# Optimization experiments

Measured on AMD Instinct MI355X. Metric: run time of the kernel, lower is better.

Reference implementation:

```python
import jax, jax.numpy as jnp
import numpy as np

B, S, E, L = 4, 4096, 1024, 64
SCALE = float(np.sqrt(L))


def setup_inputs() -> dict:
    key = jax.random.key(0)
    ks = jax.random.split(key, 7)
    x = jax.random.normal(ks[0], (B, S, E), dtype=jnp.float32)
    # causal mask: positions with mask==0 are disallowed (masked_fill semantics)
    mask = jnp.tril(jnp.ones((S, S), dtype=jnp.int32))
    # Linear params (torch Linear: y = x @ W.T + b); store as [E, L] for x @ W
    sd = 1.0 / np.sqrt(E)
    Wq = jax.random.uniform(ks[1], (E, L), jnp.float32, -sd, sd)
    Wk = jax.random.uniform(ks[2], (E, L), jnp.float32, -sd, sd)
    Wv = jax.random.uniform(ks[3], (E, L), jnp.float32, -sd, sd)
    bq = jax.random.uniform(ks[4], (L,), jnp.float32, -sd, sd)
    bk = jax.random.uniform(ks[5], (L,), jnp.float32, -sd, sd)
    bv = jax.random.uniform(ks[6], (L,), jnp.float32, -sd, sd)
    return {"x": x, "Wq": Wq, "Wk": Wk, "Wv": Wv,
            "bq": bq, "bk": bk, "bv": bv, "mask": mask}


def reference(x, Wq, Wk, Wv, bq, bk, bv, mask):
    # Q,K,V: [B, S, L]
    Q = x @ Wq + bq
    K = x @ Wk + bk
    V = x @ Wv + bv
    # scores: [B, S, S] -- naive full matrix, faithful to the original
    scores = jnp.einsum('bsl,btl->bst', Q, K) / SCALE
    scores = jnp.where(mask == 0, -jnp.inf, scores)
    attn = jax.nn.softmax(scores, axis=-1)
    return jnp.einsum('bst,btl->bsl', attn, V)
```

## Files before the change

### kernel.cpp

```cpp
#include <hip/hip_runtime.h>
#include <hip/hip_bf16.h>
#include <cstdint>

typedef __bf16 bf16_t;
typedef __bf16 bf16x8 __attribute__((ext_vector_type(8)));
typedef float f32x4 __attribute__((ext_vector_type(4)));

#define B_ 4
#define S_ 4096
#define E_ 1024
#define L_ 64

__device__ __forceinline__ f32x4 mfma16(bf16x8 a, bf16x8 b, f32x4 c) {
  return __builtin_amdgcn_mfma_f32_16x16x32_bf16(a, b, c, 0, 0, 0);
}

__device__ __forceinline__ void barrier_lds_only() {
  asm volatile("s_waitcnt lgkmcnt(0)\n\ts_barrier" ::: "memory");
}

template <int CTRL>
__device__ __forceinline__ float dpp_max_step(float x) {
  int t = __builtin_amdgcn_update_dpp(0, __float_as_int(x), CTRL, 0xF, 0xF, true);
  return fmaxf(x, __int_as_float(t));
}
template <int CTRL>
__device__ __forceinline__ float dpp_add_step(float x) {
  int t = __builtin_amdgcn_update_dpp(0, __float_as_int(x), CTRL, 0xF, 0xF, true);
  return x + __int_as_float(t);
}
__device__ __forceinline__ float dpp_reduce_max16(float x) {
  x = dpp_max_step<0x121>(x);
  x = dpp_max_step<0x122>(x);
  x = dpp_max_step<0x124>(x);
  x = dpp_max_step<0x128>(x);
  return x;
}
__device__ __forceinline__ float dpp_reduce_add16(float x) {
  x = dpp_add_step<0x121>(x);
  x = dpp_add_step<0x122>(x);
  x = dpp_add_step<0x124>(x);
  x = dpp_add_step<0x128>(x);
  return x;
}


__global__ void prep_w_kernel(const float* __restrict__ Wq, const float* __restrict__ Wk,
                              const float* __restrict__ Wv, bf16_t* __restrict__ Wf) {
  int n = blockIdx.x >> 1;
  int k0 = (blockIdx.x & 1) * 512;
  const float* W = (n < 64) ? Wq : (n < 128 ? Wk : Wv);
  int col = n & 63;
  int nt = n >> 4, lr = n & 15;
  for (int kk = threadIdx.x; kk < 512; kk += blockDim.x) {
    int k = k0 + kk;
    int kt = k >> 5, lg = (k >> 3) & 3, e = k & 7;
    Wf[((size_t)((nt * 32 + kt) * 64 + lg * 16 + lr) << 3) + e] = (bf16_t)W[(size_t)k * L_ + col];
  }
}

__global__ __launch_bounds__(512) void qkv_proj_kernel(
    const float* __restrict__ x, const bf16_t* __restrict__ Wf,
    const float* __restrict__ bq, const float* __restrict__ bk, const float* __restrict__ bv,
    bf16_t* __restrict__ Qf, bf16_t* __restrict__ Kf, bf16_t* __restrict__ Vf) {
  __shared__ __align__(16) bf16_t xbuf[2][32][136];
  bf16_t* stc = &xbuf[0][0][0];

  const int tid = threadIdx.x;
  const int w = tid >> 6, l = tid & 63;
  const int lr = l & 15, lg = l >> 4;
  const int rowgrp = w & 1, colgrp = w >> 1;
  const int m0 = blockIdx.x * 32;
  const int rot = blockIdx.x & 7;

  const int prow = tid >> 4;
  const int pcol = (tid & 15) * 8;
  float4 ra, rb;

#define QKV_CC(c) (((c) + rot) & 7)
#define QKV_LOADREG(c)                                                      \
  {                                                                         \
    const float* src = x + (size_t)(m0 + prow) * E_ + QKV_CC(c) * 128 + pcol; \
    ra = *reinterpret_cast<const float4*>(src);                             \
    rb = *reinterpret_cast<const float4*>(src + 4);                         \
  }
#define QKV_WRITE(b)                                                        \
  {                                                                         \
    bf16x8 pk;                                                              \
    pk[0] = (bf16_t)ra.x; pk[1] = (bf16_t)ra.y;                             \
    pk[2] = (bf16_t)ra.z; pk[3] = (bf16_t)ra.w;                             \
    pk[4] = (bf16_t)rb.x; pk[5] = (bf16_t)rb.y;                             \
    pk[6] = (bf16_t)rb.z; pk[7] = (bf16_t)rb.w;                             \
    *reinterpret_cast<bf16x8*>(&xbuf[(b)][prow][pcol]) = pk;                \
  }

  f32x4 acc[3];
#pragma unroll
  for (int t = 0; t < 3; ++t) acc[t] = f32x4{0.f, 0.f, 0.f, 0.f};

  QKV_LOADREG(0);
  QKV_WRITE(0);
  QKV_LOADREG(1);
  barrier_lds_only();

  for (int c = 0; c < 8; ++c) {
    const int cur = c & 1;
    const int cc = QKV_CC(c);
#pragma unroll
    for (int kt = 0; kt < 4; ++kt) {
      const int ktg = cc * 4 + kt;
      bf16x8 bfr[3];
#pragma unroll
      for (int t = 0; t < 3; ++t) {
        const int nt = colgrp * 3 + t;
        bfr[t] = *reinterpret_cast<const bf16x8*>(Wf + (((size_t)(nt * 32 + ktg) * 64 + l) << 3));
      }
      bf16x8 a = *reinterpret_cast<const bf16x8*>(
          &xbuf[cur][rowgrp * 16 + lr][kt * 32 + lg * 8]);
#pragma unroll
      for (int t = 0; t < 3; ++t) acc[t] = mfma16(a, bfr[t], acc[t]);
    }
    if (c + 1 < 8) QKV_WRITE(cur ^ 1);
    if (c + 2 < 8) QKV_LOADREG(c + 2);
    barrier_lds_only();
  }

#pragma unroll
  for (int t = 0; t < 3; ++t) {
    const int colb = colgrp * 48 + t * 16;
    const int col = colb + lr;
    const int mat = colb >> 6;
    const float* bias = (mat == 0) ? bq : (mat == 1 ? bk : bv);
    const float bb = bias[col & 63];
#pragma unroll
    for (int r = 0; r < 4; ++r) {
      const int row = rowgrp * 16 + lg * 4 + r;
      stc[row * 200 + col] = (bf16_t)(acc[t][r] + bb);
    }
  }
  __syncthreads();

  if (tid < 256) {
    const int rt = tid >> 7, ktq = (tid >> 6) & 1, lane = tid & 63;
    const int lgw = lane >> 4, lrw = lane & 15;
    const int rtg = (m0 >> 4) + rt;
    bf16x8 qv = *reinterpret_cast<const bf16x8*>(stc + (rt * 16 + lrw) * 200 + ktq * 32 + lgw * 8);
    *reinterpret_cast<bf16x8*>(Qf + (((size_t)(rtg * 2 + ktq) * 64 + lane) << 3)) = qv;
    bf16x8 kv = *reinterpret_cast<const bf16x8*>(stc + (rt * 16 + lrw) * 200 + 64 + ktq * 32 + lgw * 8);
    *reinterpret_cast<bf16x8*>(Kf + (((size_t)(rtg * 2 + ktq) * 64 + lane) << 3)) = kv;
  } else {
    const int t2 = tid - 256;
    const int vt = t2 >> 6, lane = t2 & 63;
    const int lgv = lane >> 4, lrv = lane & 15;
    const int colv = vt * 16 + lrv;
    bf16x8 vv;
#pragma unroll
    for (int e = 0; e < 8; ++e)
      vv[e] = stc[(lgv * 8 + e) * 200 + 128 + colv];
    const int batch = m0 >> 12;
    const int stg = (m0 & (S_ - 1)) >> 5;
    *reinterpret_cast<bf16x8*>(Vf + ((size_t)batch << 18) + (((size_t)(stg * 4 + vt) * 64 + lane) << 3)) = vv;
  }
#undef QKV_CC
#undef QKV_LOADREG
#undef QKV_WRITE
}

__global__ __launch_bounds__(256) void attn_kernel(
    const bf16_t* __restrict__ Qf, const bf16_t* __restrict__ Kf,
    const bf16_t* __restrict__ Vf, bf16_t* __restrict__ Opart, float* __restrict__ mlpart) {
  __shared__ __align__(16) bf16_t p_lds[4][16 * 72];
  __shared__ bf16_t od_lds[3][16][68];
  __shared__ float ml_lds[3][16][2];

  const int c = threadIdx.x >> 6, l = threadIdx.x & 63;
  const int lr = l & 15, lg = l >> 4;
  const int u = blockIdx.x;
  const int batch = u & 3;
  const int strip = (u >> 2) & 3;
  const int h = (u >> 4) & 1;
  const int qt = 63 - (u >> 5);
  const int qsi = ((u >> 5) << 4) | (u & 15);
  const int qrow = qt * 64 + strip * 16;
  bf16_t* pw = p_lds[c];

  const int rtq = batch * 256 + qt * 4 + strip;
  bf16x8 qa0 = *reinterpret_cast<const bf16x8*>(Qf + (((size_t)(rtq * 2) * 64 + l) << 3));
  bf16x8 qa1 = *reinterpret_cast<const bf16x8*>(Qf + (((size_t)(rtq * 2 + 1) * 64 + l) << 3));
  const bf16_t* Vb = Vf + ((size_t)batch << 18);

  f32x4 o[4];
  float m[4], ssum[4];
#pragma unroll
  for (int rr = 0; rr < 4; ++rr) { o[rr] = f32x4{0.f, 0.f, 0.f, 0.f}; m[rr] = -1e30f; ssum[rr] = 0.f; }

  for (int kt = 2 * c + h; kt <= qt; kt += 8) {
    const int t0 = kt * 64;
    f32x4 st[4];
#pragma unroll
    for (int cf = 0; cf < 4; ++cf) st[cf] = f32x4{0.f, 0.f, 0.f, 0.f};
#pragma unroll
    for (int cf = 0; cf < 4; ++cf) {
      const int rtk = batch * 256 + kt * 4 + cf;
      bf16x8 b0 = *reinterpret_cast<const bf16x8*>(Kf + (((size_t)(rtk * 2) * 64 + l) << 3));
      bf16x8 b1 = *reinterpret_cast<const bf16x8*>(Kf + (((size_t)(rtk * 2 + 1) * 64 + l) << 3));
      st[cf] = mfma16(qa0, b0, st[cf]);
      st[cf] = mfma16(qa1, b1, st[cf]);
    }
    const bool diag = (kt == qt);
    float p[4][4];
#pragma unroll
    for (int rr = 0; rr < 4; ++rr) {
      const int qg = qrow + lg * 4 + rr;
      float rowmax = -1e30f;
#pragma unroll
      for (int cf = 0; cf < 4; ++cf) {
        float s = st[cf][rr] * 0.125f;
        if (diag && (t0 + cf * 16 + lr) > qg) s = -1e30f;
        p[cf][rr] = s;
        rowmax = fmaxf(rowmax, s);
      }
      rowmax = dpp_reduce_max16(rowmax);
      float mnew = fmaxf(m[rr], rowmax);
      float scale = __expf(m[rr] - mnew);
      float rs = 0.f;
#pragma unroll
      for (int cf = 0; cf < 4; ++cf) {
        float e = __expf(p[cf][rr] - mnew);
        p[cf][rr] = e;
        rs += e;
      }
      rs = dpp_reduce_add16(rs);
      ssum[rr] = ssum[rr] * scale + rs;
#pragma unroll
      for (int cf = 0; cf < 4; ++cf) o[cf][rr] *= scale;
      m[rr] = mnew;
    }
#pragma unroll
    for (int rr = 0; rr < 4; ++rr)
#pragma unroll
      for (int cf = 0; cf < 4; ++cf)
        pw[(lg * 4 + rr) * 72 + cf * 16 + lr] = (bf16_t)p[cf][rr];
    bf16x8 pa0 = *reinterpret_cast<const bf16x8*>(pw + lr * 72 + lg * 8);
    bf16x8 pa1 = *reinterpret_cast<const bf16x8*>(pw + lr * 72 + 32 + lg * 8);
    const int st0 = kt * 2;
#pragma unroll
    for (int cf = 0; cf < 4; ++cf) {
      bf16x8 v0 = *reinterpret_cast<const bf16x8*>(Vb + (((size_t)((st0 * 4 + cf) * 64 + l)) << 3));
      bf16x8 v1 = *reinterpret_cast<const bf16x8*>(Vb + (((size_t)(((st0 + 1) * 4 + cf) * 64 + l)) << 3));
      o[cf] = mfma16(pa0, v0, o[cf]);
      o[cf] = mfma16(pa1, v1, o[cf]);
    }
  }

  if (c > 0) {
    if (lr == 0) {
#pragma unroll
      for (int rr = 0; rr < 4; ++rr) {
        ml_lds[c - 1][lg * 4 + rr][0] = m[rr];
        ml_lds[c - 1][lg * 4 + rr][1] = ssum[rr];
      }
    }
#pragma unroll
    for (int cf = 0; cf < 4; ++cf)
#pragma unroll
      for (int rr = 0; rr < 4; ++rr)
        od_lds[c - 1][lg * 4 + rr][cf * 16 + lr] = (bf16_t)o[cf][rr];
  }
  __syncthreads();
  if (c == 0) {
    bf16_t* Op = Opart + (size_t)(h * 1024 + qsi) * 1024;
    float* mlp = mlpart + (size_t)(h * 1024 + qsi) * 32;
#pragma unroll
    for (int rr = 0; rr < 4; ++rr) {
      const int row = lg * 4 + rr;
      float M = m[rr];
      float mv[3];
#pragma unroll
      for (int cc = 0; cc < 3; ++cc) {
        mv[cc] = ml_lds[cc][row][0];
        M = fmaxf(M, mv[cc]);
      }
      float f0 = __expf(m[rr] - M);
      float Lsum = ssum[rr] * f0;
      float fc[3];
#pragma unroll
      for (int cc = 0; cc < 3; ++cc) {
        fc[cc] = __expf(mv[cc] - M);
        Lsum += ml_lds[cc][row][1] * fc[cc];
      }
      const float invL = (Lsum > 0.f) ? (1.f / Lsum) : 0.f;
      if (lr == 0) { mlp[row * 2] = M; mlp[row * 2 + 1] = Lsum; }
#pragma unroll
      for (int cf = 0; cf < 4; ++cf) {
        float val = o[cf][rr] * f0;
#pragma unroll
        for (int cc = 0; cc < 3; ++cc)
          val += (float)od_lds[cc][row][cf * 16 + lr] * fc[cc];
        Op[row * 64 + cf * 16 + lr] = (bf16_t)(val * invL);
      }
    }
  }
}

__global__ __launch_bounds__(64) void combine_kernel(
    const bf16_t* __restrict__ Opart, const float* __restrict__ mlpart,
    float* __restrict__ out) {
  const int b = blockIdx.x;
  const int batch = b & 3, strip = (b >> 2) & 3, qt = 63 - (b >> 4);
  const int l = threadIdx.x;
  const int row = l >> 2, c0 = (l & 3) * 16;
  const float* ml0 = mlpart + ((size_t)(0 * 1024 + b) * 16 + row) * 2;
  const float* ml1 = mlpart + ((size_t)(1 * 1024 + b) * 16 + row) * 2;
  float m0 = ml0[0], l0 = ml0[1], m1 = ml1[0], l1 = ml1[1];
  float M = fmaxf(m0, m1);
  float w0 = l0 * __expf(m0 - M), w1 = l1 * __expf(m1 - M);
  float inv = 1.f / (w0 + w1);
  w0 *= inv; w1 *= inv;
  const bf16_t* O0 = Opart + (size_t)(0 * 1024 + b) * 1024 + row * 64 + c0;
  const bf16_t* O1 = Opart + (size_t)(1 * 1024 + b) * 1024 + row * 64 + c0;
  float* dst = out + ((size_t)batch * S_ + qt * 64 + strip * 16 + row) * L_ + c0;
#pragma unroll
  for (int j = 0; j < 2; ++j) {
    bf16x8 a = reinterpret_cast<const bf16x8*>(O0)[j];
    bf16x8 bb = reinterpret_cast<const bf16x8*>(O1)[j];
#pragma unroll
    for (int e = 0; e < 8; ++e)
      dst[j * 8 + e] = (float)a[e] * w0 + (float)bb[e] * w1;
  }
}

extern "C" void kernel_launch(void* const* d_in, const int* in_sizes, int n_in,
                              void* d_out, int out_size, void* d_ws, size_t ws_size,
                              hipStream_t stream) {
  (void)in_sizes; (void)n_in; (void)out_size; (void)ws_size;
  const float* x  = (const float*)d_in[0];
  const float* Wq = (const float*)d_in[1];
  const float* Wk = (const float*)d_in[2];
  const float* Wv = (const float*)d_in[3];
  const float* bq = (const float*)d_in[4];
  const float* bk = (const float*)d_in[5];
  const float* bv = (const float*)d_in[6];
  float* out = (float*)d_out;

  char* ws = (char*)d_ws;
  bf16_t* Qf  = (bf16_t*)(ws + 0);
  bf16_t* Kf  = (bf16_t*)(ws + (size_t)2 * 1024 * 1024);
  bf16_t* Vf  = (bf16_t*)(ws + (size_t)4 * 1024 * 1024);
  bf16_t* Wf  = (bf16_t*)(ws + (size_t)6 * 1024 * 1024);
  bf16_t* Opart = (bf16_t*)(ws + (size_t)7 * 1024 * 1024);
  float* mlpart = (float*)(ws + (size_t)12 * 1024 * 1024);

  hipLaunchKernelGGL(prep_w_kernel, dim3(384), dim3(256), 0, stream, Wq, Wk, Wv, Wf);
  hipLaunchKernelGGL(qkv_proj_kernel, dim3(16384 / 32), dim3(512), 0, stream,
                     x, Wf, bq, bk, bv, Qf, Kf, Vf);
  hipLaunchKernelGGL(attn_kernel, dim3(2048), dim3(256), 0, stream,
                     Qf, Kf, Vf, Opart, mlpart);
  hipLaunchKernelGGL(combine_kernel, dim3(1024), dim3(64), 0, stream,
                     Opart, mlpart, out);
}
```

Before: 59.39 us.

## Pre-cast x to bf16 in MFMA fragment layout via separate kernel

Adds an xcast kernel that converts x from fp32 to bf16 and writes it in the MFMA A-fragment layout. The QKV projection then reads A fragments straight from global memory, with no LDS double buffering and no per-chunk barriers. This removes the cast and sync work from the projection's inner loop. In exchange it adds a kernel launch and an extra 32MB round trip for the bf16 copy of x (read 64MB fp32, write 32MB, then read 32MB again), which is likely to cost more than it saves for a memory-bound stage.

```diff
diff --git a/kernel.cpp b/kernel.cpp
--- a/kernel.cpp
+++ b/kernel.cpp
@@ -13,10 +13,6 @@
 
 __device__ __forceinline__ f32x4 mfma16(bf16x8 a, bf16x8 b, f32x4 c) {
   return __builtin_amdgcn_mfma_f32_16x16x32_bf16(a, b, c, 0, 0, 0);
-}
-
-__device__ __forceinline__ void barrier_lds_only() {
-  asm volatile("s_waitcnt lgkmcnt(0)\n\ts_barrier" ::: "memory");
 }
 
 template <int CTRL>
@@ -44,6 +40,39 @@
   return x;
 }
 
+
+__global__ __launch_bounds__(256) void xcast_kernel(
+    const float* __restrict__ x, bf16_t* __restrict__ xf) {
+  __shared__ __align__(16) bf16_t xs[16][1048];
+  const int tid = threadIdx.x;
+  const int m0 = blockIdx.x * 16;
+  {
+    const float* xb = x + (size_t)m0 * E_;
+#pragma unroll
+    for (int p = 0; p < 8; ++p) {
+      const int g = p * 256 + tid;
+      const int row = g >> 7, col = (g & 127) * 8;
+      float4 u0 = *reinterpret_cast<const float4*>(xb + (size_t)row * E_ + col);
+      float4 u1 = *reinterpret_cast<const float4*>(xb + (size_t)row * E_ + col + 4);
+      bf16x8 pk;
+      pk[0] = (bf16_t)u0.x; pk[1] = (bf16_t)u0.y; pk[2] = (bf16_t)u0.z; pk[3] = (bf16_t)u0.w;
+      pk[4] = (bf16_t)u1.x; pk[5] = (bf16_t)u1.y; pk[6] = (bf16_t)u1.z; pk[7] = (bf16_t)u1.w;
+      *reinterpret_cast<bf16x8*>(&xs[row][col]) = pk;
+    }
+  }
+  __syncthreads();
+  {
+    const int rt = m0 >> 4;
+#pragma unroll
+    for (int i = 0; i < 8; ++i) {
+      const int idx = i * 256 + tid;
+      const int lane = idx & 63, kt = idx >> 6;
+      const int lrw = lane & 15, lgw = lane >> 4;
+      bf16x8 v = *reinterpret_cast<const bf16x8*>(&xs[lrw][kt * 32 + lgw * 8]);
+      *reinterpret_cast<bf16x8*>(xf + (((size_t)(rt * 32 + kt) * 64 + lane) << 3)) = v;
+    }
+  }
+}
 
 __global__ void prep_w_kernel(const float* __restrict__ Wq, const float* __restrict__ Wk,
                               const float* __restrict__ Wv, bf16_t* __restrict__ Wf) {
@@ -60,69 +89,32 @@
 }
 
 __global__ __launch_bounds__(512) void qkv_proj_kernel(
-    const float* __restrict__ x, const bf16_t* __restrict__ Wf,
+    const bf16_t* __restrict__ xf, const bf16_t* __restrict__ Wf,
     const float* __restrict__ bq, const float* __restrict__ bk, const float* __restrict__ bv,
     bf16_t* __restrict__ Qf, bf16_t* __restrict__ Kf, bf16_t* __restrict__ Vf) {
-  __shared__ __align__(16) bf16_t xbuf[2][32][136];
-  bf16_t* stc = &xbuf[0][0][0];
+  __shared__ __align__(16) bf16_t stc[32 * 200];
 
   const int tid = threadIdx.x;
   const int w = tid >> 6, l = tid & 63;
   const int lr = l & 15, lg = l >> 4;
   const int rowgrp = w & 1, colgrp = w >> 1;
   const int m0 = blockIdx.x * 32;
-  const int rot = blockIdx.x & 7;
-
-  const int prow = tid >> 4;
-  const int pcol = (tid & 15) * 8;
-  float4 ra, rb;
-
-#define QKV_CC(c) (((c) + rot) & 7)
-#define QKV_LOADREG(c)                                                      \
-  {                                                                         \
-    const float* src = x + (size_t)(m0 + prow) * E_ + QKV_CC(c) * 128 + pcol; \
-    ra = *reinterpret_cast<const float4*>(src);                             \
-    rb = *reinterpret_cast<const float4*>(src + 4);                         \
-  }
-#define QKV_WRITE(b)                                                        \
-  {                                                                         \
-    bf16x8 pk;                                                              \
-    pk[0] = (bf16_t)ra.x; pk[1] = (bf16_t)ra.y;                             \
-    pk[2] = (bf16_t)ra.z; pk[3] = (bf16_t)ra.w;                             \
-    pk[4] = (bf16_t)rb.x; pk[5] = (bf16_t)rb.y;                             \
-    pk[6] = (bf16_t)rb.z; pk[7] = (bf16_t)rb.w;                             \
-    *reinterpret_cast<bf16x8*>(&xbuf[(b)][prow][pcol]) = pk;                \
-  }
+  const int rtg = (m0 >> 4) + rowgrp;
 
   f32x4 acc[3];
 #pragma unroll
   for (int t = 0; t < 3; ++t) acc[t] = f32x4{0.f, 0.f, 0.f, 0.f};
 
-  QKV_LOADREG(0);
-  QKV_WRITE(0);
-  QKV_LOADREG(1);
-  barrier_lds_only();
-
-  for (int c = 0; c < 8; ++c) {
-    const int cur = c & 1;
-    const int cc = QKV_CC(c);
-#pragma unroll
-    for (int kt = 0; kt < 4; ++kt) {
-      const int ktg = cc * 4 + kt;
-      bf16x8 bfr[3];
-#pragma unroll
-      for (int t = 0; t < 3; ++t) {
-        const int nt = colgrp * 3 + t;
-        bfr[t] = *reinterpret_cast<const bf16x8*>(Wf + (((size_t)(nt * 32 + ktg) * 64 + l) << 3));
-      }
-      bf16x8 a = *reinterpret_cast<const bf16x8*>(
-          &xbuf[cur][rowgrp * 16 + lr][kt * 32 + lg * 8]);
-#pragma unroll
-      for (int t = 0; t < 3; ++t) acc[t] = mfma16(a, bfr[t], acc[t]);
-    }
-    if (c + 1 < 8) QKV_WRITE(cur ^ 1);
-    if (c + 2 < 8) QKV_LOADREG(c + 2);
-    barrier_lds_only();
+  const bf16_t* xa = xf + (((size_t)rtg * 32) * 64 + l) * 8;
+#pragma unroll 4
+  for (int ktg = 0; ktg < 32; ++ktg) {
+    bf16x8 a = *reinterpret_cast<const bf16x8*>(xa + ((size_t)ktg * 64) * 8);
+#pragma unroll
+    for (int t = 0; t < 3; ++t) {
+      const int nt = colgrp * 3 + t;
+      bf16x8 b = *reinterpret_cast<const bf16x8*>(Wf + (((size_t)(nt * 32 + ktg) * 64 + l) << 3));
+      acc[t] = mfma16(a, b, acc[t]);
+    }
   }
 
 #pragma unroll
@@ -143,11 +135,11 @@
   if (tid < 256) {
     const int rt = tid >> 7, ktq = (tid >> 6) & 1, lane = tid & 63;
     const int lgw = lane >> 4, lrw = lane & 15;
-    const int rtg = (m0 >> 4) + rt;
+    const int rtq2 = (m0 >> 4) + rt;
     bf16x8 qv = *reinterpret_cast<const bf16x8*>(stc + (rt * 16 + lrw) * 200 + ktq * 32 + lgw * 8);
-    *reinterpret_cast<bf16x8*>(Qf + (((size_t)(rtg * 2 + ktq) * 64 + lane) << 3)) = qv;
+    *reinterpret_cast<bf16x8*>(Qf + (((size_t)(rtq2 * 2 + ktq) * 64 + lane) << 3)) = qv;
     bf16x8 kv = *reinterpret_cast<const bf16x8*>(stc + (rt * 16 + lrw) * 200 + 64 + ktq * 32 + lgw * 8);
-    *reinterpret_cast<bf16x8*>(Kf + (((size_t)(rtg * 2 + ktq) * 64 + lane) << 3)) = kv;
+    *reinterpret_cast<bf16x8*>(Kf + (((size_t)(rtq2 * 2 + ktq) * 64 + lane) << 3)) = kv;
   } else {
     const int t2 = tid - 256;
     const int vt = t2 >> 6, lane = t2 & 63;
@@ -161,9 +153,6 @@
     const int stg = (m0 & (S_ - 1)) >> 5;
     *reinterpret_cast<bf16x8*>(Vf + ((size_t)batch << 18) + (((size_t)(stg * 4 + vt) * 64 + lane) << 3)) = vv;
   }
-#undef QKV_CC
-#undef QKV_LOADREG
-#undef QKV_WRITE
 }
 
 __global__ __launch_bounds__(256) void attn_kernel(
@@ -350,10 +339,12 @@
   bf16_t* Wf  = (bf16_t*)(ws + (size_t)6 * 1024 * 1024);
   bf16_t* Opart = (bf16_t*)(ws + (size_t)7 * 1024 * 1024);
   float* mlpart = (float*)(ws + (size_t)12 * 1024 * 1024);
-
+  bf16_t* xf  = (bf16_t*)(ws + (size_t)16 * 1024 * 1024);
+
+  hipLaunchKernelGGL(xcast_kernel, dim3(1024), dim3(256), 0, stream, x, xf);
   hipLaunchKernelGGL(prep_w_kernel, dim3(384), dim3(256), 0, stream, Wq, Wk, Wv, Wf);
   hipLaunchKernelGGL(qkv_proj_kernel, dim3(16384 / 32), dim3(512), 0, stream,
-                     x, Wf, bq, bk, bv, Qf, Kf, Vf);
+                     xf, Wf, bq, bk, bv, Qf, Kf, Vf);
   hipLaunchKernelGGL(attn_kernel, dim3(2048), dim3(256), 0, stream,
                      Qf, Kf, Vf, Opart, mlpart);
   hipLaunchKernelGGL(combine_kernel, dim3(1024), dim3(64), 0, stream,
```

Measured after the change: 80.95 us. 1.36x slower.
